# Optimization experiments

Measured on AMD Instinct MI355X. Metric: run time of the kernel, lower is better.

## Reference

```python
import jax, jax.numpy as jnp
import numpy as np

NOT_EPSILON = 1.0
B, Q, K, T = 2, 512, 512, 256  # batch, num queries, num keys, dims


def swishmax(x, axis):
    # x * exp(x - max) / (sum(|x * exp(x - max)|) + 1)
    xexp = x * jnp.exp(x - jnp.max(x, axis=axis, keepdims=True))
    return xexp / (jnp.sum(jnp.abs(xexp), axis=axis, keepdims=True) + NOT_EPSILON)


def setup_inputs() -> dict:
    key = jax.random.key(0)
    ks = jax.random.split(key, 8)
    s = 1.0 / np.sqrt(T)
    return {
        "query_tokens": jax.random.normal(ks[0], (B, Q, T), jnp.float32),
        "key_tokens": jax.random.normal(ks[1], (B, K, T), jnp.float32),
        "value_tokens": jax.random.normal(ks[2], (B, K, T), jnp.float32),
        "Wk": jax.random.normal(ks[3], (T, T), jnp.float32) * s,
        "Wq": jax.random.normal(ks[4], (T, T), jnp.float32) * s,
        "Wva": jax.random.normal(ks[5], (T, T), jnp.float32) * s,
        "Wal": jax.random.normal(ks[6], (T, T), jnp.float32) * s,
        "Wvo": jax.random.normal(ks[7], (T, T), jnp.float32) * s,
    }


def reference(query_tokens, key_tokens, value_tokens, Wk, Wq, Wva, Wal, Wvo):
    # torch nn.Linear: y = x @ W.T (no biases)
    k = jnp.einsum('bkt,ut->bku', key_tokens, Wk)      # [B,K,T]
    q = jnp.einsum('bqt,ut->bqu', query_tokens, Wq)    # [B,Q,T]
    # elementwise outer product over token pairs: [B,K,Q,T]
    raw = k[:, :, None, :] * q[:, None, :, :]
    logits = jnp.einsum('bkqt,ut->bkqu', raw, Wal)     # [B,K,Q,T]
    scale = swishmax(logits, axis=-2)                  # normalize over Q
    v = jnp.einsum('bkt,ut->bku', value_tokens, Wva)   # [B,K,T]
    values_scaled = v[:, :, None, :] * scale           # [B,K,Q,T]
    value_sum = values_scaled.sum(axis=-3)             # sum over K -> [B,Q,T]
    return jnp.einsum('bqt,ut->bqu', value_sum, Wvo)   # [B,Q,T]
```

## Files before the change

kernel.cpp:

```cpp
#include <hip/hip_runtime.h>
#include <cstdint>


typedef short bf16x8 __attribute__((ext_vector_type(8)));
typedef float f32x4  __attribute__((ext_vector_type(4)));

__device__ inline float bf2f(short s) {
  return __uint_as_float(((unsigned)(unsigned short)s) << 16);
}
__device__ inline unsigned packrn(float lo, float hi) {
  return __builtin_amdgcn_perm(__float_as_uint(hi) + 0x8000u,
                               __float_as_uint(lo) + 0x8000u, 0x07060302u);
}
__device__ inline unsigned encM(float f) {
  unsigned k = (unsigned)__float_as_int(f);
  return (k & 0x80000000u) ? ~k : (k | 0x80000000u);
}
__device__ inline float decM(unsigned k) {
  int i = (k & 0x80000000u) ? (int)(k ^ 0x80000000u) : (int)~k;
  return __int_as_float(i);
}

#define GEMM_BODY32(X, W, K0, K1)                                               \
  __shared__ __align__(16) float As[16][36];                                    \
  __shared__ __align__(16) float Ws[16][68];                                    \
  const int tid = threadIdx.x;                                                  \
  const int tx4 = (tid & 15) * 4;                                               \
  const int ty2 = (tid >> 4) * 2;                                               \
  const int m0 = blockIdx.x * 32, u0 = blockIdx.y * 64;                         \
  const int lmi = tid >> 2, lc4 = (tid & 3) * 4;                                \
  const bool hasA = tid < 128;                                                  \
  float4 xa, wb;                                                                \
  if (hasA) xa = *(const float4*)&(X)[(size_t)(m0 + lmi) * 256 + (K0) + lc4];   \
  wb = *(const float4*)&(W)[(size_t)(u0 + lmi) * 256 + (K0) + lc4];             \
  float c[2][4] = {};                                                           \
  _Pragma("unroll 1")                                                           \
  for (int t0 = (K0); t0 < (K1); t0 += 16) {                                    \
    __syncthreads();                                                            \
    if (hasA) {                                                                 \
      As[lc4 + 0][lmi] = xa.x; As[lc4 + 1][lmi] = xa.y;                         \
      As[lc4 + 2][lmi] = xa.z; As[lc4 + 3][lmi] = xa.w;                         \
    }                                                                           \
    Ws[lc4 + 0][lmi] = wb.x; Ws[lc4 + 1][lmi] = wb.y;                           \
    Ws[lc4 + 2][lmi] = wb.z; Ws[lc4 + 3][lmi] = wb.w;                           \
    __syncthreads();                                                            \
    if (t0 + 16 < (K1)) {                                                       \
      if (hasA) xa = *(const float4*)&(X)[(size_t)(m0 + lmi) * 256 + t0 + 16 + lc4]; \
      wb = *(const float4*)&(W)[(size_t)(u0 + lmi) * 256 + t0 + 16 + lc4];      \
    }                                                                           \
    _Pragma("unroll")                                                           \
    for (int t = 0; t < 16; ++t) {                                              \
      const float2 a = *(const float2*)&As[t][ty2];                             \
      const float4 w = *(const float4*)&Ws[t][tx4];                             \
      c[0][0] += a.x*w.x; c[0][1] += a.x*w.y; c[0][2] += a.x*w.z; c[0][3] += a.x*w.w; \
      c[1][0] += a.y*w.x; c[1][1] += a.y*w.y; c[1][2] += a.y*w.z; c[1][3] += a.y*w.w; \
    }                                                                           \
  }

__global__ __launch_bounds__(256) void proj3(
    const float* __restrict__ key, const float* __restrict__ value,
    const float* __restrict__ query, const float* __restrict__ Wk,
    const float* __restrict__ Wq, const float* __restrict__ Wva,
    const float* __restrict__ Wal, float* __restrict__ kproj,
    float* __restrict__ vproj, short* __restrict__ qpF,
    short* __restrict__ WalF, float* __restrict__ vsum,
    float* __restrict__ outz)
{
  const int z = blockIdx.z;
  if (z == 3) {
    const int p = blockIdx.x * 4 + blockIdx.y;
    if (p >= 64) return;
    const int t256 = threadIdx.x;
#pragma unroll
    for (int e = 0; e < 4; ++e) {
      const int d = p * 1024 + t256 * 4 + e;
      const int j = d & 7, uu = (d >> 3) & 31, c8g = d >> 8;
      const int ucx = c8g >> 5, cc = c8g & 31;
      const float v = Wal[(ucx * 32 + uu) * 256 + cc * 8 + j];
      WalF[d] = (short)packrn(v, v);
    }
    float4* vz = (float4*)(vsum + p * 4096);
    float4* oz = (float4*)(outz + p * 4096);
#pragma unroll
    for (int e = 0; e < 4; ++e) {
      vz[t256 * 4 + e] = make_float4(0.f, 0.f, 0.f, 0.f);
      oz[t256 * 4 + e] = make_float4(0.f, 0.f, 0.f, 0.f);
    }
    return;
  }
  const float* X = (z == 0) ? key : (z == 1) ? value : query;
  const float* W = (z == 0) ? Wk  : (z == 1) ? Wva   : Wq;
  GEMM_BODY32(X, W, 0, 256);
  if (z == 2) {
    const int tbase = u0 + tx4;
    const int ks = tbase >> 5, l4f = (tbase & 31) >> 3, j0 = tbase & 7;
#pragma unroll
    for (int i = 0; i < 2; ++i) {
      const int m = m0 + ty2 + i;
      const int bb = m >> 9, q = m & 511;
      const int g = q >> 4, l15q = q & 15;
      const size_t idx = ((size_t)(((bb * 32 + g) * 8 + ks) * 64) + l4f * 16 + l15q) * 8 + j0;
      uint2 s; s.x = packrn(c[i][0], c[i][1]); s.y = packrn(c[i][2], c[i][3]);
      *(uint2*)&qpF[idx] = s;
    }
  } else {
    float* C = (z == 0) ? kproj : vproj;
#pragma unroll
    for (int i = 0; i < 2; ++i)
      *(float4*)&C[(size_t)(m0 + ty2 + i) * 256 + u0 + tx4] =
          make_float4(c[i][0], c[i][1], c[i][2], c[i][3]);
  }
}

__global__ __launch_bounds__(256) void gemm_out(
    const float* __restrict__ X, const float* __restrict__ W, float* __restrict__ out)
{
  const int kh = blockIdx.z * 128;
  GEMM_BODY32(X, W, kh, kh + 128);
#pragma unroll
  for (int i = 0; i < 2; ++i)
#pragma unroll
    for (int j = 0; j < 4; ++j)
      atomicAdd(&out[(size_t)(m0 + ty2 + i) * 256 + u0 + tx4 + j], c[i][j]);
}

union Frag { bf16x8 v; unsigned u[4]; };

__global__ __launch_bounds__(512, 2) void kernelC(
    const short* __restrict__ qpF, const float* __restrict__ kproj,
    const float* __restrict__ vproj, const short* __restrict__ WalF,
    float* __restrict__ vsum)
{
  __shared__ __align__(16) short W2F[2][8192];
  __shared__ float vpS[32 * 33];
  __shared__ unsigned statM[96];
  __shared__ float statS[96];

  const int kt = blockIdx.x, uc = blockIdx.y, b = blockIdx.z;
  const int u0 = uc * 32, k0 = kt * 32;
  const int tid = threadIdx.x;
  const int lane = tid & 63, w = tid >> 6;
  const int l15 = lane & 15, l4 = lane >> 4;
  const int uu = tid & 31, c8 = tid >> 5;

  if (tid < 96) { statM[tid] = 0u; statS[tid] = 0.f; }
  {
    const int kk = tid >> 4, uu2 = (tid & 15) * 2;
    const float2 v2 = *(const float2*)&vproj[(size_t)(b * 512 + k0 + kk) * 256 + u0 + uu2];
    vpS[kk * 33 + uu2] = v2.x; vpS[kk * 33 + uu2 + 1] = v2.y;
  }

  float wl0[8], wl1[8];
  {
    const bf16x8 w0 = *(const bf16x8*)&WalF[((size_t)(uc * 32 + c8) * 32 + uu) * 8];
    const bf16x8 w1 = *(const bf16x8*)&WalF[((size_t)(uc * 32 + c8 + 16) * 32 + uu) * 8];
#pragma unroll
    for (int j = 0; j < 8; ++j) { wl0[j] = bf2f(w0[j]); wl1[j] = bf2f(w1[j]); }
  }

  const short* qbase = qpF + (size_t)b * 131072;
  Frag qa[4][8];
#pragma unroll
  for (int qg = 0; qg < 4; ++qg)
#pragma unroll
    for (int ks = 0; ks < 8; ++ks) {
      qa[qg][ks].v = *(const bf16x8*)&qbase[(((size_t)(w * 4 + qg) * 8 + ks) * 64 + lane) * 8];
      asm volatile("" : "+v"(qa[qg][ks].u[0]), "+v"(qa[qg][ks].u[1]),
                        "+v"(qa[qg][ks].u[2]), "+v"(qa[qg][ks].u[3]));
    }

  const int fb = (l4 * 32 + l15) * 8;
  const float* kq = &kproj[(long)(b * 512 + k0) * 256 + c8 * 8];

  {
    const f32x4 a0 = *(const f32x4*)(kq);
    const f32x4 a1 = *(const f32x4*)(kq + 4);
    const f32x4 b0 = *(const f32x4*)(kq + 128);
    const f32x4 b1 = *(const f32x4*)(kq + 132);
    uint4 st;
    st.x = packrn(wl0[0] * a0[0], wl0[1] * a0[1]);
    st.y = packrn(wl0[2] * a0[2], wl0[3] * a0[3]);
    st.z = packrn(wl0[4] * a1[0], wl0[5] * a1[1]);
    st.w = packrn(wl0[6] * a1[2], wl0[7] * a1[3]);
    *(uint4*)&W2F[0][(c8 * 32 + uu) * 8] = st;
    st.x = packrn(wl1[0] * b0[0], wl1[1] * b0[1]);
    st.y = packrn(wl1[2] * b0[2], wl1[3] * b0[3]);
    st.z = packrn(wl1[4] * b1[0], wl1[5] * b1[1]);
    st.w = packrn(wl1[6] * b1[2], wl1[7] * b1[3]);
    *(uint4*)&W2F[0][((c8 + 16) * 32 + uu) * 8] = st;
  }
  __syncthreads();

  const f32x4 z4 = {0.f, 0.f, 0.f, 0.f};
  f32x4 acc[4][2] = {z4, z4, z4, z4, z4, z4, z4, z4};

#pragma unroll 1
  for (int kk = 0; kk < 32; ++kk) {
    const int cs = kk & 1, ss = kk % 3;

    f32x4 a0, a1, b0, b1;
    if (kk < 31) {
      const float* kn = kq + (size_t)(kk + 1) * 256;
      a0 = *(const f32x4*)(kn);
      a1 = *(const f32x4*)(kn + 4);
      b0 = *(const f32x4*)(kn + 128);
      b1 = *(const f32x4*)(kn + 132);
    }

    f32x4 lg[4][2] = {z4, z4, z4, z4, z4, z4, z4, z4};
#pragma unroll
    for (int ks = 0; ks < 8; ++ks) {
      const bf16x8 f0 = *(const bf16x8*)&W2F[cs][fb + ks * 1024];
      const bf16x8 f1 = *(const bf16x8*)&W2F[cs][fb + ks * 1024 + 128];
#pragma unroll
      for (int qg = 0; qg < 4; ++qg) {
        lg[qg][0] = __builtin_amdgcn_mfma_f32_16x16x32_bf16(qa[qg][ks].v, f0, lg[qg][0], 0, 0, 0);
        lg[qg][1] = __builtin_amdgcn_mfma_f32_16x16x32_bf16(qa[qg][ks].v, f1, lg[qg][1], 0, 0, 0);
      }
    }

    if (kk < 31) {
      uint4 st;
      st.x = packrn(wl0[0] * a0[0], wl0[1] * a0[1]);
      st.y = packrn(wl0[2] * a0[2], wl0[3] * a0[3]);
      st.z = packrn(wl0[4] * a1[0], wl0[5] * a1[1]);
      st.w = packrn(wl0[6] * a1[2], wl0[7] * a1[3]);
      *(uint4*)&W2F[cs ^ 1][(c8 * 32 + uu) * 8] = st;
      st.x = packrn(wl1[0] * b0[0], wl1[1] * b0[1]);
      st.y = packrn(wl1[2] * b0[2], wl1[3] * b0[3]);
      st.z = packrn(wl1[4] * b1[0], wl1[5] * b1[1]);
      st.w = packrn(wl1[6] * b1[2], wl1[7] * b1[3]);
      *(uint4*)&W2F[cs ^ 1][((c8 + 16) * 32 + uu) * 8] = st;
    }

#pragma unroll
    for (int qg = 0; qg < 4; ++qg)
      asm volatile("" : "+v"(lg[qg][0]), "+v"(lg[qg][1]));

    float Mv[2], Sv[2];
#pragma unroll
    for (int ug = 0; ug < 2; ++ug) {
      const float m0q = fmaxf(fmaxf(fmaxf(lg[0][ug][0], lg[0][ug][1]), lg[0][ug][2]), lg[0][ug][3]);
      const float m1q = fmaxf(fmaxf(fmaxf(lg[1][ug][0], lg[1][ug][1]), lg[1][ug][2]), lg[1][ug][3]);
      const float m2q = fmaxf(fmaxf(fmaxf(lg[2][ug][0], lg[2][ug][1]), lg[2][ug][2]), lg[2][ug][3]);
      const float m3q = fmaxf(fmaxf(fmaxf(lg[3][ug][0], lg[3][ug][1]), lg[3][ug][2]), lg[3][ug][3]);
      float m = fmaxf(fmaxf(fmaxf(m0q, m1q), m2q), m3q);
      float sq[4];
#pragma unroll
      for (int qg = 0; qg < 4; ++qg) {
        float p0 = lg[qg][ug][0] * __expf(lg[qg][ug][0]);
        float p1 = lg[qg][ug][1] * __expf(lg[qg][ug][1]);
        float p2 = lg[qg][ug][2] * __expf(lg[qg][ug][2]);
        float p3 = lg[qg][ug][3] * __expf(lg[qg][ug][3]);
        lg[qg][ug][0] = p0; lg[qg][ug][1] = p1;
        lg[qg][ug][2] = p2; lg[qg][ug][3] = p3;
        sq[qg] = (fabsf(p0) + fabsf(p1)) + (fabsf(p2) + fabsf(p3));
      }
      float s = (sq[0] + sq[1]) + (sq[2] + sq[3]);
      m = fmaxf(m, __shfl_xor(m, 16));
      m = fmaxf(m, __shfl_xor(m, 32));
      s += __shfl_xor(s, 16);
      s += __shfl_xor(s, 32);
      Mv[ug] = m; Sv[ug] = s;
    }
    if (l4 == 0) {
      atomicMax(&statM[ss * 32 + l15],      encM(Mv[0]));
      atomicMax(&statM[ss * 32 + 16 + l15], encM(Mv[1]));
      atomicAdd(&statS[ss * 32 + l15],      Sv[0]);
      atomicAdd(&statS[ss * 32 + 16 + l15], Sv[1]);
    }
    __syncthreads();

#pragma unroll
    for (int ug = 0; ug < 2; ++ug) {
      const int ui = ug * 16 + l15;
      const float M = decM(statM[ss * 32 + ui]);
      const float S = statS[ss * 32 + ui];
      const float em = __expf(-M);
      const float g = vpS[kk * 33 + ui] * em * __builtin_amdgcn_rcpf(fmaf(S, em, 1.0f));
#pragma unroll
      for (int qg = 0; qg < 4; ++qg)
#pragma unroll
        for (int i = 0; i < 4; ++i)
          acc[qg][ug][i] = fmaf(g, lg[qg][ug][i], acc[qg][ug][i]);
    }
#pragma unroll
    for (int qg = 0; qg < 4; ++qg)
      asm volatile("" : "+v"(acc[qg][0]), "+v"(acc[qg][1]));

    const int rs = (kk + 2) % 3;
    if (tid < 32) { statM[rs * 32 + tid] = 0u; statS[rs * 32 + tid] = 0.f; }
  }

#pragma unroll
  for (int qg = 0; qg < 4; ++qg)
#pragma unroll
    for (int ug = 0; ug < 2; ++ug)
#pragma unroll
      for (int i = 0; i < 4; ++i)
        atomicAdd(&vsum[(size_t)(b * 512 + w * 64 + qg * 16 + l4 * 4 + i) * 256 +
                        u0 + ug * 16 + l15],
                  acc[qg][ug][i]);
}

extern "C" void kernel_launch(void* const* d_in, const int* in_sizes, int n_in,
                              void* d_out, int out_size, void* d_ws, size_t ws_size,
                              hipStream_t stream) {
  const float* query = (const float*)d_in[0];
  const float* key   = (const float*)d_in[1];
  const float* value = (const float*)d_in[2];
  const float* Wk    = (const float*)d_in[3];
  const float* Wq    = (const float*)d_in[4];
  const float* Wva   = (const float*)d_in[5];
  const float* Wal   = (const float*)d_in[6];
  const float* Wvo   = (const float*)d_in[7];
  float* ws = (float*)d_ws;

  float* kproj = ws;
  float* vproj = kproj + 262144;
  float* vsum  = vproj + 262144;
  short* qpF   = (short*)(vsum + 262144);
  short* WalF  = qpF + 262144;
  float* out   = (float*)d_out;

  proj3<<<dim3(32, 4, 4), 256, 0, stream>>>(key, value, query, Wk, Wq, Wva, Wal,
                                            kproj, vproj, qpF, WalF, vsum, out);
  kernelC<<<dim3(16, 8, 2), 512, 0, stream>>>(qpF, kproj, vproj, WalF, vsum);
  gemm_out<<<dim3(32, 4, 2), 256, 0, stream>>>(vsum, Wvo, out);
}
```

Measured before the change: 186.4 us.

## Switch logits MFMA to 32x32x16 tiles and simplify swishmax stats reduction

Replaces the 16x16x32 bf16 MFMA tiling of the per-key logits with 32x32x16 MFMAs, which changes the fragment layouts of the packed query and Wal buffers and the LDS W2F layout. The swishmax normalisation is rewritten to track the max of exp(x) directly, with positive floats compared as unsigned ints, so the order-preserving encode/decode and the extra exp(-M) drop out. The cross-lane reduction shrinks from two shuffles to one. The goal is fewer MFMA issues, less shuffle and atomic work per iteration, and fewer reduction steps, in exchange for a different register footprint and a denominator computed as S+max(e) instead of S*exp(-M)+1.

After: 176.4 us. -5.3%, faster.

```diff
diff --git a/kernel.cpp b/kernel.cpp
--- a/kernel.cpp
+++ b/kernel.cpp
@@ -4,6 +4,7 @@
 
 typedef short bf16x8 __attribute__((ext_vector_type(8)));
 typedef float f32x4  __attribute__((ext_vector_type(4)));
+typedef float f32x16 __attribute__((ext_vector_type(16)));
 
 __device__ inline float bf2f(short s) {
   return __uint_as_float(((unsigned)(unsigned short)s) << 16);
@@ -11,14 +12,6 @@
 __device__ inline unsigned packrn(float lo, float hi) {
   return __builtin_amdgcn_perm(__float_as_uint(hi) + 0x8000u,
                                __float_as_uint(lo) + 0x8000u, 0x07060302u);
-}
-__device__ inline unsigned encM(float f) {
-  unsigned k = (unsigned)__float_as_int(f);
-  return (k & 0x80000000u) ? ~k : (k | 0x80000000u);
-}
-__device__ inline float decM(unsigned k) {
-  int i = (k & 0x80000000u) ? (int)(k ^ 0x80000000u) : (int)~k;
-  return __int_as_float(i);
 }
 
 #define GEMM_BODY32(X, W, K0, K1)                                               \
@@ -74,9 +67,7 @@
 #pragma unroll
     for (int e = 0; e < 4; ++e) {
       const int d = p * 1024 + t256 * 4 + e;
-      const int j = d & 7, uu = (d >> 3) & 31, c8g = d >> 8;
-      const int ucx = c8g >> 5, cc = c8g & 31;
-      const float v = Wal[(ucx * 32 + uu) * 256 + cc * 8 + j];
+      const float v = Wal[d];
       WalF[d] = (short)packrn(v, v);
     }
     float4* vz = (float4*)(vsum + p * 4096);
@@ -93,13 +84,15 @@
   GEMM_BODY32(X, W, 0, 256);
   if (z == 2) {
     const int tbase = u0 + tx4;
-    const int ks = tbase >> 5, l4f = (tbase & 31) >> 3, j0 = tbase & 7;
+    const int ts = tbase >> 4, khalf = (tbase >> 3) & 1, j0 = tbase & 7;
 #pragma unroll
     for (int i = 0; i < 2; ++i) {
       const int m = m0 + ty2 + i;
       const int bb = m >> 9, q = m & 511;
-      const int g = q >> 4, l15q = q & 15;
-      const size_t idx = ((size_t)(((bb * 32 + g) * 8 + ks) * 64) + l4f * 16 + l15q) * 8 + j0;
+      const int g32 = q >> 5, row = q & 31;
+      const int lane = khalf * 32 + row;
+      const size_t idx =
+          (((size_t)(bb * 16 + g32) * 16 + ts) * 64 + lane) * 8 + j0;
       uint2 s; s.x = packrn(c[i][0], c[i][1]); s.y = packrn(c[i][2], c[i][3]);
       *(uint2*)&qpF[idx] = s;
     }
@@ -124,7 +117,8 @@
       atomicAdd(&out[(size_t)(m0 + ty2 + i) * 256 + u0 + tx4 + j], c[i][j]);
 }
 
-union Frag { bf16x8 v; unsigned u[4]; };
+union Frag  { bf16x8 v; unsigned u[4]; };
+union Acc16 { f32x16 v; f32x4 f4[4]; };
 
 __global__ __launch_bounds__(512, 2) void kernelC(
     const short* __restrict__ qpF, const float* __restrict__ kproj,
@@ -140,8 +134,8 @@
   const int u0 = uc * 32, k0 = kt * 32;
   const int tid = threadIdx.x;
   const int lane = tid & 63, w = tid >> 6;
-  const int l15 = lane & 15, l4 = lane >> 4;
-  const int uu = tid & 31, c8 = tid >> 5;
+  const int ul = lane & 31;
+  const int tsb = tid >> 5, ub = tid & 31;
 
   if (tid < 96) { statM[tid] = 0u; statS[tid] = 0.f; }
   {
@@ -152,71 +146,68 @@
 
   float wl0[8], wl1[8];
   {
-    const bf16x8 w0 = *(const bf16x8*)&WalF[((size_t)(uc * 32 + c8) * 32 + uu) * 8];
-    const bf16x8 w1 = *(const bf16x8*)&WalF[((size_t)(uc * 32 + c8 + 16) * 32 + uu) * 8];
+    const bf16x8 w0 = *(const bf16x8*)&WalF[(size_t)(uc * 32 + ub) * 256 + tsb * 16];
+    const bf16x8 w1 = *(const bf16x8*)&WalF[(size_t)(uc * 32 + ub) * 256 + tsb * 16 + 8];
 #pragma unroll
     for (int j = 0; j < 8; ++j) { wl0[j] = bf2f(w0[j]); wl1[j] = bf2f(w1[j]); }
   }
 
   const short* qbase = qpF + (size_t)b * 131072;
-  Frag qa[4][8];
-#pragma unroll
-  for (int qg = 0; qg < 4; ++qg)
-#pragma unroll
-    for (int ks = 0; ks < 8; ++ks) {
-      qa[qg][ks].v = *(const bf16x8*)&qbase[(((size_t)(w * 4 + qg) * 8 + ks) * 64 + lane) * 8];
-      asm volatile("" : "+v"(qa[qg][ks].u[0]), "+v"(qa[qg][ks].u[1]),
-                        "+v"(qa[qg][ks].u[2]), "+v"(qa[qg][ks].u[3]));
-    }
-
-  const int fb = (l4 * 32 + l15) * 8;
-  const float* kq = &kproj[(long)(b * 512 + k0) * 256 + c8 * 8];
+  Frag qa[2][16];
+#pragma unroll
+  for (int qt = 0; qt < 2; ++qt)
+#pragma unroll
+    for (int ts = 0; ts < 16; ++ts) {
+      qa[qt][ts].v = *(const bf16x8*)&qbase[(((size_t)(w * 2 + qt) * 16 + ts) * 64 + lane) * 8];
+      asm volatile("" : "+v"(qa[qt][ts].u[0]), "+v"(qa[qt][ts].u[1]),
+                        "+v"(qa[qt][ts].u[2]), "+v"(qa[qt][ts].u[3]));
+    }
+
+  const int fb = lane * 8;
+  const float* kq = &kproj[(long)(b * 512 + k0) * 256 + tsb * 16];
 
   {
     const f32x4 a0 = *(const f32x4*)(kq);
     const f32x4 a1 = *(const f32x4*)(kq + 4);
-    const f32x4 b0 = *(const f32x4*)(kq + 128);
-    const f32x4 b1 = *(const f32x4*)(kq + 132);
+    const f32x4 a2 = *(const f32x4*)(kq + 8);
+    const f32x4 a3 = *(const f32x4*)(kq + 12);
     uint4 st;
     st.x = packrn(wl0[0] * a0[0], wl0[1] * a0[1]);
     st.y = packrn(wl0[2] * a0[2], wl0[3] * a0[3]);
     st.z = packrn(wl0[4] * a1[0], wl0[5] * a1[1]);
     st.w = packrn(wl0[6] * a1[2], wl0[7] * a1[3]);
-    *(uint4*)&W2F[0][(c8 * 32 + uu) * 8] = st;
-    st.x = packrn(wl1[0] * b0[0], wl1[1] * b0[1]);
-    st.y = packrn(wl1[2] * b0[2], wl1[3] * b0[3]);
-    st.z = packrn(wl1[4] * b1[0], wl1[5] * b1[1]);
-    st.w = packrn(wl1[6] * b1[2], wl1[7] * b1[3]);
-    *(uint4*)&W2F[0][((c8 + 16) * 32 + uu) * 8] = st;
+    *(uint4*)&W2F[0][(tsb * 64 + ub) * 8] = st;
+    st.x = packrn(wl1[0] * a2[0], wl1[1] * a2[1]);
+    st.y = packrn(wl1[2] * a2[2], wl1[3] * a2[3]);
+    st.z = packrn(wl1[4] * a3[0], wl1[5] * a3[1]);
+    st.w = packrn(wl1[6] * a3[2], wl1[7] * a3[3]);
+    *(uint4*)&W2F[0][(tsb * 64 + 32 + ub) * 8] = st;
   }
   __syncthreads();
 
-  const f32x4 z4 = {0.f, 0.f, 0.f, 0.f};
-  f32x4 acc[4][2] = {z4, z4, z4, z4, z4, z4, z4, z4};
+  Acc16 acc[2];
+  acc[0].v = 0.f; acc[1].v = 0.f;
 
 #pragma unroll 1
   for (int kk = 0; kk < 32; ++kk) {
     const int cs = kk & 1, ss = kk % 3;
 
-    f32x4 a0, a1, b0, b1;
+    f32x4 a0, a1, a2, a3;
     if (kk < 31) {
       const float* kn = kq + (size_t)(kk + 1) * 256;
       a0 = *(const f32x4*)(kn);
       a1 = *(const f32x4*)(kn + 4);
-      b0 = *(const f32x4*)(kn + 128);
-      b1 = *(const f32x4*)(kn + 132);
-    }
-
-    f32x4 lg[4][2] = {z4, z4, z4, z4, z4, z4, z4, z4};
-#pragma unroll
-    for (int ks = 0; ks < 8; ++ks) {
-      const bf16x8 f0 = *(const bf16x8*)&W2F[cs][fb + ks * 1024];
-      const bf16x8 f1 = *(const bf16x8*)&W2F[cs][fb + ks * 1024 + 128];
-#pragma unroll
-      for (int qg = 0; qg < 4; ++qg) {
-        lg[qg][0] = __builtin_amdgcn_mfma_f32_16x16x32_bf16(qa[qg][ks].v, f0, lg[qg][0], 0, 0, 0);
-        lg[qg][1] = __builtin_amdgcn_mfma_f32_16x16x32_bf16(qa[qg][ks].v, f1, lg[qg][1], 0, 0, 0);
-      }
+      a2 = *(const f32x4*)(kn + 8);
+      a3 = *(const f32x4*)(kn + 12);
+    }
+
+    Acc16 lg[2];
+    lg[0].v = 0.f; lg[1].v = 0.f;
+#pragma unroll
+    for (int ts = 0; ts < 16; ++ts) {
+      const bf16x8 f = *(const bf16x8*)&W2F[cs][ts * 512 + fb];
+      lg[0].v = __builtin_amdgcn_mfma_f32_32x32x16_bf16(qa[0][ts].v, f, lg[0].v, 0, 0, 0);
+      lg[1].v = __builtin_amdgcn_mfma_f32_32x32x16_bf16(qa[1][ts].v, f, lg[1].v, 0, 0, 0);
     }
 
     if (kk < 31) {
@@ -225,82 +216,70 @@
       st.y = packrn(wl0[2] * a0[2], wl0[3] * a0[3]);
       st.z = packrn(wl0[4] * a1[0], wl0[5] * a1[1]);
       st.w = packrn(wl0[6] * a1[2], wl0[7] * a1[3]);
-      *(uint4*)&W2F[cs ^ 1][(c8 * 32 + uu) * 8] = st;
-      st.x = packrn(wl1[0] * b0[0], wl1[1] * b0[1]);
-      st.y = packrn(wl1[2] * b0[2], wl1[3] * b0[3]);
-      st.z = packrn(wl1[4] * b1[0], wl1[5] * b1[1]);
-      st.w = packrn(wl1[6] * b1[2], wl1[7] * b1[3]);
-      *(uint4*)&W2F[cs ^ 1][((c8 + 16) * 32 + uu) * 8] = st;
-    }
-
-#pragma unroll
-    for (int qg = 0; qg < 4; ++qg)
-      asm volatile("" : "+v"(lg[qg][0]), "+v"(lg[qg][1]));
-
-    float Mv[2], Sv[2];
-#pragma unroll
-    for (int ug = 0; ug < 2; ++ug) {
-      const float m0q = fmaxf(fmaxf(fmaxf(lg[0][ug][0], lg[0][ug][1]), lg[0][ug][2]), lg[0][ug][3]);
-      const float m1q = fmaxf(fmaxf(fmaxf(lg[1][ug][0], lg[1][ug][1]), lg[1][ug][2]), lg[1][ug][3]);
-      const float m2q = fmaxf(fmaxf(fmaxf(lg[2][ug][0], lg[2][ug][1]), lg[2][ug][2]), lg[2][ug][3]);
-      const float m3q = fmaxf(fmaxf(fmaxf(lg[3][ug][0], lg[3][ug][1]), lg[3][ug][2]), lg[3][ug][3]);
-      float m = fmaxf(fmaxf(fmaxf(m0q, m1q), m2q), m3q);
-      float sq[4];
-#pragma unroll
-      for (int qg = 0; qg < 4; ++qg) {
-        float p0 = lg[qg][ug][0] * __expf(lg[qg][ug][0]);
-        float p1 = lg[qg][ug][1] * __expf(lg[qg][ug][1]);
-        float p2 = lg[qg][ug][2] * __expf(lg[qg][ug][2]);
-        float p3 = lg[qg][ug][3] * __expf(lg[qg][ug][3]);
-        lg[qg][ug][0] = p0; lg[qg][ug][1] = p1;
-        lg[qg][ug][2] = p2; lg[qg][ug][3] = p3;
-        sq[qg] = (fabsf(p0) + fabsf(p1)) + (fabsf(p2) + fabsf(p3));
+      *(uint4*)&W2F[cs ^ 1][(tsb * 64 + ub) * 8] = st;
+      st.x = packrn(wl1[0] * a2[0], wl1[1] * a2[1]);
+      st.y = packrn(wl1[2] * a2[2], wl1[3] * a2[3]);
+      st.z = packrn(wl1[4] * a3[0], wl1[5] * a3[1]);
+      st.w = packrn(wl1[6] * a3[2], wl1[7] * a3[3]);
+      *(uint4*)&W2F[cs ^ 1][(tsb * 64 + 32 + ub) * 8] = st;
+    }
+
+#pragma unroll
+    for (int qt = 0; qt < 2; ++qt)
+      asm volatile("" : "+v"(lg[qt].f4[0]), "+v"(lg[qt].f4[1]),
+                        "+v"(lg[qt].f4[2]), "+v"(lg[qt].f4[3]));
+
+    float em[4] = {0.f, 0.f, 0.f, 0.f};
+    float sp[4] = {0.f, 0.f, 0.f, 0.f};
+#pragma unroll
+    for (int qt = 0; qt < 2; ++qt)
+#pragma unroll
+      for (int r = 0; r < 16; ++r) {
+        const float x = lg[qt].f4[r >> 2][r & 3];
+        const float e = __expf(x);
+        const float p = x * e;
+        lg[qt].f4[r >> 2][r & 3] = p;
+        em[r & 3] = fmaxf(em[r & 3], e);
+        sp[r & 3] += fabsf(p);
       }
-      float s = (sq[0] + sq[1]) + (sq[2] + sq[3]);
-      m = fmaxf(m, __shfl_xor(m, 16));
-      m = fmaxf(m, __shfl_xor(m, 32));
-      s += __shfl_xor(s, 16);
-      s += __shfl_xor(s, 32);
-      Mv[ug] = m; Sv[ug] = s;
-    }
-    if (l4 == 0) {
-      atomicMax(&statM[ss * 32 + l15],      encM(Mv[0]));
-      atomicMax(&statM[ss * 32 + 16 + l15], encM(Mv[1]));
-      atomicAdd(&statS[ss * 32 + l15],      Sv[0]);
-      atomicAdd(&statS[ss * 32 + 16 + l15], Sv[1]);
+    float EM = fmaxf(fmaxf(em[0], em[1]), fmaxf(em[2], em[3]));
+    float S  = (sp[0] + sp[1]) + (sp[2] + sp[3]);
+    EM = fmaxf(EM, __shfl_xor(EM, 32));
+    S += __shfl_xor(S, 32);
+    if (lane < 32) {
+      atomicMax(&statM[ss * 32 + ul], __float_as_uint(EM));
+      atomicAdd(&statS[ss * 32 + ul], S);
     }
     __syncthreads();
 
-#pragma unroll
-    for (int ug = 0; ug < 2; ++ug) {
-      const int ui = ug * 16 + l15;
-      const float M = decM(statM[ss * 32 + ui]);
-      const float S = statS[ss * 32 + ui];
-      const float em = __expf(-M);
-      const float g = vpS[kk * 33 + ui] * em * __builtin_amdgcn_rcpf(fmaf(S, em, 1.0f));
-#pragma unroll
-      for (int qg = 0; qg < 4; ++qg)
-#pragma unroll
-        for (int i = 0; i < 4; ++i)
-          acc[qg][ug][i] = fmaf(g, lg[qg][ug][i], acc[qg][ug][i]);
-    }
-#pragma unroll
-    for (int qg = 0; qg < 4; ++qg)
-      asm volatile("" : "+v"(acc[qg][0]), "+v"(acc[qg][1]));
+    {
+      const float EMf = __uint_as_float(statM[ss * 32 + ul]);
+      const float Sf  = statS[ss * 32 + ul];
+      const float g = vpS[kk * 33 + ul] * __builtin_amdgcn_rcpf(Sf + EMf);
+#pragma unroll
+      for (int qt = 0; qt < 2; ++qt)
+#pragma unroll
+        for (int r = 0; r < 16; ++r)
+          acc[qt].f4[r >> 2][r & 3] =
+              fmaf(g, lg[qt].f4[r >> 2][r & 3], acc[qt].f4[r >> 2][r & 3]);
+    }
+#pragma unroll
+    for (int qt = 0; qt < 2; ++qt)
+      asm volatile("" : "+v"(acc[qt].f4[0]), "+v"(acc[qt].f4[1]),
+                        "+v"(acc[qt].f4[2]), "+v"(acc[qt].f4[3]));
 
     const int rs = (kk + 2) % 3;
     if (tid < 32) { statM[rs * 32 + tid] = 0u; statS[rs * 32 + tid] = 0.f; }
   }
 
 #pragma unroll
-  for (int qg = 0; qg < 4; ++qg)
-#pragma unroll
-    for (int ug = 0; ug < 2; ++ug)
-#pragma unroll
-      for (int i = 0; i < 4; ++i)
-        atomicAdd(&vsum[(size_t)(b * 512 + w * 64 + qg * 16 + l4 * 4 + i) * 256 +
-                        u0 + ug * 16 + l15],
-                  acc[qg][ug][i]);
+  for (int qt = 0; qt < 2; ++qt)
+#pragma unroll
+    for (int r = 0; r < 16; ++r) {
+      const int q = w * 64 + qt * 32 + (r & 3) + 8 * (r >> 2) + 4 * (lane >> 5);
+      atomicAdd(&vsum[(size_t)(b * 512 + q) * 256 + u0 + ul],
+                acc[qt].f4[r >> 2][r & 3]);
+    }
 }
 
 extern "C" void kernel_launch(void* const* d_in, const int* in_sizes, int n_in,
```
